# Optimization experiments

Measured on AMD Instinct MI355X. Metric: run time of the kernel, lower is better.

Reference implementation:

```python
import jax, jax.numpy as jnp
import numpy as np

N_NODES = 10000
N_EDGES = 25000
D_FEAT = 128

def setup_inputs() -> dict:
    key = jax.random.key(0)
    k1, k2, k3 = jax.random.split(key, 3)
    x = jax.random.normal(k1, (N_NODES, D_FEAT), dtype=jnp.float32)
    edge_attr = jax.random.normal(k2, (N_EDGES, D_FEAT), dtype=jnp.float32)
    edge_index = jax.random.randint(k3, (2, N_EDGES), 0, N_NODES, dtype=jnp.int64)
    return {"x": x, "edge_attr": edge_attr, "edge_index": edge_index}

def reference(x, edge_attr, edge_index):
    # lg_node_idx: [E, 2] (src, dst) pairs; each original edge becomes a line-graph node
    lg_node_idx = edge_index.T
    # gather endpoint features and average -> [E, d]
    new_x = x[lg_node_idx].mean(axis=1)
    # stack([x, edge_attr], dim=2).mean(dim=2) == elementwise average
    new_x = (new_x + edge_attr) * 0.5
    col0 = lg_node_idx[:, 0]  # src of each edge
    col1 = lg_node_idx[:, 1]  # dst of each edge
    # edge i -> edge j connected iff dst(i) == src(j) and src(i) != dst(j)
    mask = (col1[:, None] == col0[None, :]) & (col0[:, None] != col1[None, :])  # [E, E]
    rows, cols = jnp.nonzero(mask)  # data-dependent size; eager (non-jit) reference
    lg_edge_index = jnp.stack([rows, cols], axis=0)  # [2, E_lg]
    # attr of line-graph edge = feature of shared node's incoming edge's dst entry
    lg_edge_attr_idx = lg_node_idx[rows][:, 1]
    lg_edge_attr = new_x[lg_edge_attr_idx]
    return new_x, lg_edge_index, lg_edge_attr
```

## Files before the change

### kernel.cpp

```cpp
#include <hip/hip_runtime.h>

#define NN 10000
#define NE 25000
#define DF 128
#define SB 256
#define NBLK ((NE + SB - 1) / SB)

__global__ void k_newx_init(const float* __restrict__ x, const float* __restrict__ ea,
                            const int* __restrict__ c0, const int* __restrict__ c1,
                            float* __restrict__ out, int* __restrict__ head,
                            int* __restrict__ gFlag) {
    int tid = blockIdx.x * blockDim.x + threadIdx.x;
    if (tid < NN) head[tid] = -1;
    if (tid < NBLK) gFlag[tid] = 0;
    if (tid >= NE * 32) return;
    int e = tid >> 5, q = tid & 31;
    int u = c0[e], v = c1[e];
    float4 a = ((const float4*)(x + (size_t)u * DF))[q];
    float4 b = ((const float4*)(x + (size_t)v * DF))[q];
    float4 c = ((const float4*)(ea + (size_t)e * DF))[q];
    float4 r;
    r.x = ((a.x + b.x) * 0.5f + c.x) * 0.5f;
    r.y = ((a.y + b.y) * 0.5f + c.y) * 0.5f;
    r.z = ((a.z + b.z) * 0.5f + c.z) * 0.5f;
    r.w = ((a.w + b.w) * 0.5f + c.w) * 0.5f;
    ((float4*)(out + (size_t)e * DF))[q] = r;
}

__global__ void k_link(const int* __restrict__ c0,
                       int* __restrict__ head, int* __restrict__ nxt) {
    int j = blockIdx.x * blockDim.x + threadIdx.x;
    if (j >= NE) return;
    nxt[j] = atomicExch(&head[c0[j]], j);
}

__global__ __launch_bounds__(SB) void k_cnt_scan(const int* __restrict__ c0,
                                                 const int* __restrict__ c1,
                                                 const int* __restrict__ head,
                                                 const int* __restrict__ nxt,
                                                 int* __restrict__ gFlag,
                                                 int* __restrict__ rowStart) {
    __shared__ int sc[SB];
    __shared__ int sr[SB];
    int b = blockIdx.x, t = threadIdx.x;
    int i = b * SB + t;
    int cnt = 0;
    if (i < NE) {
        int u = c0[i], v = c1[i];
        for (int j = head[v]; j != -1; j = nxt[j])
            if (c1[j] != u) ++cnt;
    }
    sc[t] = cnt;
    __syncthreads();
    for (int off = 1; off < SB; off <<= 1) {
        int add = (t >= off) ? sc[t - off] : 0;
        __syncthreads();
        sc[t] += add;
        __syncthreads();
    }
    int blockSum = sc[SB - 1];
    if (t == 0) atomicExch(&gFlag[b], blockSum + 1);
    int val = 0;
    if (t < b) {
        int v2;
        do { v2 = atomicAdd(&gFlag[t], 0); } while (v2 == 0);
        val = v2 - 1;
    }
    sr[t] = val;
    __syncthreads();
    for (int off = SB / 2; off > 0; off >>= 1) {
        if (t < off) sr[t] += sr[t + off];
        __syncthreads();
    }
    int base = sr[0];
    if (i < NE) rowStart[i] = base + sc[t] - cnt;
    if (b == NBLK - 1 && t == 0) rowStart[NE] = base + blockSum;
}

__global__ void k_emit(const float* __restrict__ newx,
                       const int* __restrict__ c0, const int* __restrict__ c1,
                       const int* __restrict__ head, const int* __restrict__ nxt,
                       const int* __restrict__ rowStart,
                       float* __restrict__ outRows, float* __restrict__ outCols,
                       float* __restrict__ outAttr) {
    int gtid = blockIdx.x * blockDim.x + threadIdx.x;
    int i = gtid >> 6, lane = gtid & 63;
    if (i >= NE) return;
    int base = rowStart[i];
    int cnt  = rowStart[i + 1] - base;
    if (cnt == 0) return;
    int u = c0[i], v = c1[i];

    int myj = -1, B = 0;
    for (int j = head[v]; j != -1; j = nxt[j], ++B)
        if (B == lane) myj = j;

    if (B <= 64) {
        int myc1 = (myj >= 0) ? c1[myj] : -1;
        bool keep = (myj >= 0) && (myc1 != u);
        int rank = 0;
        for (int q = 0; q < B; ++q) {
            int jq = __shfl(myj, q);
            int cq = __shfl(myc1, q);
            if (cq != u && jq < myj) ++rank;
        }
        if (keep) {
            outRows[base + rank] = (float)i;
            outCols[base + rank] = (float)myj;
        }
    } else {
        int pos = 0;
        for (int j = head[v]; j != -1; j = nxt[j], ++pos) {
            if ((pos & 63) != lane) continue;
            if (c1[j] == u) continue;
            int rank = 0;
            for (int j2 = head[v]; j2 != -1; j2 = nxt[j2])
                rank += (c1[j2] != u && j2 < j) ? 1 : 0;
            outRows[base + rank] = (float)i;
            outCols[base + rank] = (float)j;
        }
    }

    float4 val = ((const float4*)(newx + (size_t)v * DF))[lane & 31];
    for (int tt = (lane >> 5); tt < cnt; tt += 2)
        ((float4*)(outAttr + (size_t)(base + tt) * DF))[lane & 31] = val;
}


extern "C" void kernel_launch(void* const* d_in, const int* in_sizes, int n_in,
                              void* d_out, int out_size, void* d_ws, size_t ws_size,
                              hipStream_t stream) {
    const float* x  = (const float*)d_in[0];
    const float* ea = (const float*)d_in[1];
    const int*   ei = (const int*)d_in[2];
    const int* c0 = ei;
    const int* c1 = ei + NE;

    float* out = (float*)d_out;
    int E_lg = (out_size - NE * DF) / (DF + 2);
    if (E_lg < 0) E_lg = 0;

    float* out_newx = out;
    float* out_rows = out + (size_t)NE * DF;
    float* out_cols = out_rows + E_lg;
    float* out_attr = out_cols + E_lg;

    int* ws       = (int*)d_ws;
    int* head     = ws;
    int* nxt      = head + NN;
    int* rowStart = nxt + NE;
    int* gFlag    = rowStart + NE + 1;

    k_newx_init<<<(NE * 32 + 255) / 256, 256, 0, stream>>>(x, ea, c0, c1, out_newx,
                                                           head, gFlag);
    k_link<<<(NE + 255) / 256, 256, 0, stream>>>(c0, head, nxt);
    k_cnt_scan<<<NBLK, SB, 0, stream>>>(c0, c1, head, nxt, gFlag, rowStart);
    k_emit<<<(NE * 64 + 255) / 256, 256, 0, stream>>>(out_newx, c0, c1, head, nxt,
                                                      rowStart, out_rows, out_cols, out_attr);
}
```

Baseline: 38.62 us.

## Move new_x computation into scan kernel as extra blocks to overlap work

The init kernel now only resets head and flags. The bandwidth-heavy new_x averaging moves into the count/scan kernel, running as extra blocks after the scan blocks. The goal is to hide the latency-bound, serially chained decoupled scan behind the memory-bound new_x work and to shorten the first kernel. Scan blocks get the low block indices, so the spin-wait chain should not deadlock, though scheduling changes could affect how much the two kinds of work actually overlap.

```diff
diff --git a/kernel.cpp b/kernel.cpp
--- a/kernel.cpp
+++ b/kernel.cpp
@@ -5,26 +5,12 @@
 #define DF 128
 #define SB 256
 #define NBLK ((NE + SB - 1) / SB)
+#define NEWXB ((NE * 32 + SB - 1) / SB)
 
-__global__ void k_newx_init(const float* __restrict__ x, const float* __restrict__ ea,
-                            const int* __restrict__ c0, const int* __restrict__ c1,
-                            float* __restrict__ out, int* __restrict__ head,
-                            int* __restrict__ gFlag) {
+__global__ void k_init(int* __restrict__ head, int* __restrict__ gFlag) {
     int tid = blockIdx.x * blockDim.x + threadIdx.x;
     if (tid < NN) head[tid] = -1;
     if (tid < NBLK) gFlag[tid] = 0;
-    if (tid >= NE * 32) return;
-    int e = tid >> 5, q = tid & 31;
-    int u = c0[e], v = c1[e];
-    float4 a = ((const float4*)(x + (size_t)u * DF))[q];
-    float4 b = ((const float4*)(x + (size_t)v * DF))[q];
-    float4 c = ((const float4*)(ea + (size_t)e * DF))[q];
-    float4 r;
-    r.x = ((a.x + b.x) * 0.5f + c.x) * 0.5f;
-    r.y = ((a.y + b.y) * 0.5f + c.y) * 0.5f;
-    r.z = ((a.z + b.z) * 0.5f + c.z) * 0.5f;
-    r.w = ((a.w + b.w) * 0.5f + c.w) * 0.5f;
-    ((float4*)(out + (size_t)e * DF))[q] = r;
 }
 
 __global__ void k_link(const int* __restrict__ c0,
@@ -34,15 +20,36 @@
     nxt[j] = atomicExch(&head[c0[j]], j);
 }
 
-__global__ __launch_bounds__(SB) void k_cnt_scan(const int* __restrict__ c0,
-                                                 const int* __restrict__ c1,
-                                                 const int* __restrict__ head,
-                                                 const int* __restrict__ nxt,
-                                                 int* __restrict__ gFlag,
-                                                 int* __restrict__ rowStart) {
+__global__ __launch_bounds__(SB) void k_scan_newx(const float* __restrict__ x,
+                                                  const float* __restrict__ ea,
+                                                  const int* __restrict__ c0,
+                                                  const int* __restrict__ c1,
+                                                  const int* __restrict__ head,
+                                                  const int* __restrict__ nxt,
+                                                  int* __restrict__ gFlag,
+                                                  int* __restrict__ rowStart,
+                                                  float* __restrict__ out) {
+    int b = blockIdx.x, t = threadIdx.x;
+
+    if (b >= NBLK) {
+        int tid = (b - NBLK) * SB + t;
+        if (tid >= NE * 32) return;
+        int e = tid >> 5, q = tid & 31;
+        int u = c0[e], v = c1[e];
+        float4 a  = ((const float4*)(x + (size_t)u * DF))[q];
+        float4 bb = ((const float4*)(x + (size_t)v * DF))[q];
+        float4 c  = ((const float4*)(ea + (size_t)e * DF))[q];
+        float4 r;
+        r.x = ((a.x + bb.x) * 0.5f + c.x) * 0.5f;
+        r.y = ((a.y + bb.y) * 0.5f + c.y) * 0.5f;
+        r.z = ((a.z + bb.z) * 0.5f + c.z) * 0.5f;
+        r.w = ((a.w + bb.w) * 0.5f + c.w) * 0.5f;
+        ((float4*)(out + (size_t)e * DF))[q] = r;
+        return;
+    }
+
     __shared__ int sc[SB];
     __shared__ int sr[SB];
-    int b = blockIdx.x, t = threadIdx.x;
     int i = b * SB + t;
     int cnt = 0;
     if (i < NE) {
@@ -151,10 +158,10 @@
     int* rowStart = nxt + NE;
     int* gFlag    = rowStart + NE + 1;
 
-    k_newx_init<<<(NE * 32 + 255) / 256, 256, 0, stream>>>(x, ea, c0, c1, out_newx,
-                                                           head, gFlag);
-    k_link<<<(NE + 255) / 256, 256, 0, stream>>>(c0, head, nxt);
-    k_cnt_scan<<<NBLK, SB, 0, stream>>>(c0, c1, head, nxt, gFlag, rowStart);
-    k_emit<<<(NE * 64 + 255) / 256, 256, 0, stream>>>(out_newx, c0, c1, head, nxt,
-                                                      rowStart, out_rows, out_cols, out_attr);
+    k_init<<<(NN + SB - 1) / SB, SB, 0, stream>>>(head, gFlag);
+    k_link<<<(NE + SB - 1) / SB, SB, 0, stream>>>(c0, head, nxt);
+    k_scan_newx<<<NBLK + NEWXB, SB, 0, stream>>>(x, ea, c0, c1, head, nxt,
+                                                 gFlag, rowStart, out_newx);
+    k_emit<<<(NE * 64 + SB - 1) / SB, SB, 0, stream>>>(out_newx, c0, c1, head, nxt,
+                                                       rowStart, out_rows, out_cols, out_attr);
 }
```

Result: slower. 40.34 us (+4.5%).
